# Optimization experiments

Measured on AMD Instinct MI355X. Metric: run time of the kernel, lower is better.

The kernel has to match this reference:

```python
import jax, jax.numpy as jnp
import numpy as np

B, R, C, OUT, IN = 64, 2048, 32, 32, 16
ROUTING_ITERS = 3


def squash(s, axis=-1):
    s_norm = jnp.linalg.norm(s, axis=axis, keepdims=True)
    scale = s_norm ** 2 / (1.0 + s_norm ** 2)
    return scale * s / (s_norm + 1e-8)


def setup_inputs() -> dict:
    key = jax.random.key(0)
    k1, k2 = jax.random.split(key)
    x = jax.random.normal(k1, (B, R, IN), dtype=jnp.float32)
    W = jax.random.normal(k2, (1, R, C, OUT, IN), dtype=jnp.float32)
    return {"x": x, "W": W}


def reference(x, W):
    # u_hat[b,r,c,o] = sum_i W[r,c,o,i] * x[b,r,i]
    u_hat = jnp.einsum('rcoi,bri->brco', W[0], x)  # [B,R,C,OUT]
    b = jnp.zeros((x.shape[0], R, C), dtype=x.dtype)
    v = None
    for i in range(ROUTING_ITERS):
        c = jax.nn.softmax(b, axis=2)[..., None]       # [B,R,C,1]
        s = jnp.sum(c * u_hat, axis=1)                 # [B,C,OUT]
        v = squash(s)                                  # [B,C,OUT]
        if i < ROUTING_ITERS - 1:
            b = b + jnp.einsum('brco,bco->brc', u_hat, v)
    return v
```

## Files before the change

kernel.cpp:

```cpp
#include <hip/hip_runtime.h>


#define Bn 64
#define Rn 2048
#define Cn 32
#define On 32
#define In 16
#define RCH 16
#define NRC2 (Rn / RCH)
#define NG 4

typedef _Float16 half4v __attribute__((ext_vector_type(4)));
typedef float floatx4 __attribute__((ext_vector_type(4)));

__global__ __launch_bounds__(256)
void wconv(const float* __restrict__ W, _Float16* __restrict__ Wh) {
    const size_t i = ((size_t)blockIdx.x * 256 + threadIdx.x) * 8;
    const float4 a = *(const float4*)(W + i);
    const float4 b = *(const float4*)(W + i + 4);
    union { _Float16 h[8]; uint4 u; } pk;
    pk.h[0] = (_Float16)a.x; pk.h[1] = (_Float16)a.y;
    pk.h[2] = (_Float16)a.z; pk.h[3] = (_Float16)a.w;
    pk.h[4] = (_Float16)b.x; pk.h[5] = (_Float16)b.y;
    pk.h[6] = (_Float16)b.z; pk.h[7] = (_Float16)b.w;
    *(uint4*)(Wh + i) = pk.u;
}

template <int PHASE>
__global__ __launch_bounds__(512, 2)
void upass(const float* __restrict__ x, const _Float16* __restrict__ Wh,
           const float* __restrict__ vroute, float* __restrict__ s_part) {
    const int tid  = threadIdx.x;
    const int w    = tid >> 6;
    const int lane = tid & 63;
    const int q    = lane >> 4;
    const int bl   = lane & 15;

    const int L  = blockIdx.x;
    const int bg = (L >> 3) & 3;
    const int rc = (L & 7) | ((L >> 5) << 3);
    const int b0 = bg * 16;

    __shared__ __attribute__((aligned(16))) _Float16 xs[RCH * 16 * 20];
    __shared__ __attribute__((aligned(16))) float vs[(PHASE > 0) ? 16 * 1028 : 4];
    __shared__ __attribute__((aligned(16))) float sums[2][16][8];

#pragma unroll
    for (int k = 0; k < 2; ++k) {
        const int u  = tid + k * 512;
        const int rr = u >> 6, bb = (u >> 2) & 15, iq = u & 3;
        const float4 xv = *(const float4*)(x + (size_t)(b0 + bb) * (Rn * In) +
                                           (size_t)(rc * RCH + rr) * In + iq * 4);
        union { _Float16 h[4]; uint2 u2; } p;
        p.h[0] = (_Float16)xv.x; p.h[1] = (_Float16)xv.y;
        p.h[2] = (_Float16)xv.z; p.h[3] = (_Float16)xv.w;
        *(uint2*)(xs + (rr * 16 + bb) * 20 + iq * 4) = p.u2;
    }
    if constexpr (PHASE > 0) {
#pragma unroll
        for (int k = 0; k < 8; ++k) {
            const int u = tid + k * 512;
            const int bb = u >> 8, off = (u & 255) * 4;
            const float4 vv = *(const float4*)(vroute + (size_t)(b0 + bb) * 1024 + off);
            *(float4*)(vs + bb * 1028 + off) = vv;
        }
    }
    __syncthreads();

    floatx4 accS[8];
#pragma unroll
    for (int m = 0; m < 8; ++m) accS[m] = (floatx4){0.f, 0.f, 0.f, 0.f};

    for (int rr = 0; rr < RCH; ++rr) {
        const int r = rc * RCH + rr;
        const _Float16* Wr = Wh + ((size_t)r * 1024 + w * 128 + bl) * 16 + 4 * q;
        half4v a[8];
#pragma unroll
        for (int m = 0; m < 8; ++m) a[m] = *(const half4v*)(Wr + m * 256);
        const half4v bf = *(const half4v*)(xs + (rr * 16 + bl) * 20 + 4 * q);

        if constexpr (PHASE == 0) {
#pragma unroll
            for (int m = 0; m < 8; ++m)
                accS[m] = __builtin_amdgcn_mfma_f32_16x16x16f16(a[m], bf, accS[m], 0, 0, 0);
        } else {
            floatx4 D[8];
#pragma unroll
            for (int m = 0; m < 8; ++m)
                D[m] = __builtin_amdgcn_mfma_f32_16x16x16f16(
                           a[m], bf, (floatx4){0.f, 0.f, 0.f, 0.f}, 0, 0, 0);

            float e[4], se = 0.f;
#pragma unroll
            for (int t = 0; t < 4; ++t) {
                const int ct = w * 4 + t;
                const float* vp = vs + bl * 1028 + ct * 32 + 4 * q;
                const floatx4 v0 = *(const floatx4*)(vp);
                const floatx4 v1 = *(const floatx4*)(vp + 16);
                float lp = D[2*t].x * v0.x + D[2*t].y * v0.y +
                           D[2*t].z * v0.z + D[2*t].w * v0.w +
                           D[2*t+1].x * v1.x + D[2*t+1].y * v1.y +
                           D[2*t+1].z * v1.z + D[2*t+1].w * v1.w;
                lp += __shfl_xor(lp, 16, 64);
                lp += __shfl_xor(lp, 32, 64);
                e[t] = __expf(lp);
                se += e[t];
            }
            if (lane < 16) sums[rr & 1][bl][w] = se;
            __syncthreads();
            const floatx4 s0 = *(const floatx4*)(&sums[rr & 1][bl][0]);
            const floatx4 s1 = *(const floatx4*)(&sums[rr & 1][bl][4]);
            const float tot = s0.x + s0.y + s0.z + s0.w +
                              s1.x + s1.y + s1.z + s1.w;
            const float winv = __builtin_amdgcn_rcpf(tot);
#pragma unroll
            for (int t = 0; t < 4; ++t) {
                const float wt = e[t] * winv;
                accS[2*t]   += wt * D[2*t];
                accS[2*t+1] += wt * D[2*t+1];
            }
        }
    }

    const size_t sb = (((size_t)rc * 64 + b0 + bl)) * 1024 + w * 128 + 4 * q;
#pragma unroll
    for (int m = 0; m < 8; ++m)
        *(floatx4*)(s_part + sb + m * 16) = accS[m];
}

__global__ __launch_bounds__(256)
void reduce_all(const float* __restrict__ sp, float* __restrict__ s2) {
    const int b = blockIdx.x, t = threadIdx.x;
    floatx4 acc = (floatx4){0.f, 0.f, 0.f, 0.f};
    for (int k = 0; k < NRC2; ++k)
        acc += *(const floatx4*)(sp + ((size_t)k * 64 + b) * 1024 + t * 4);
    *(floatx4*)(s2 + (size_t)b * 1024 + t * 4) = acc;
}

__global__ __launch_bounds__(256)
void squash_v(const float* __restrict__ s2, float scale,
              float* __restrict__ vout, const float* __restrict__ vprev,
              float* __restrict__ vsum) {
    const int b = blockIdx.x, t = threadIdx.x;
    const int c = t >> 3, j = t & 7;
    floatx4 s = *(const floatx4*)(s2 + (size_t)b * 1024 + c * 32 + j * 4);
    s *= scale;
    float n2 = s.x * s.x + s.y * s.y + s.z * s.z + s.w * s.w;
    n2 += __shfl_xor(n2, 1, 64);
    n2 += __shfl_xor(n2, 2, 64);
    n2 += __shfl_xor(n2, 4, 64);
    const float norm = sqrtf(n2);
    const float f = (n2 / (1.f + n2)) / (norm + 1e-8f);
    const floatx4 vv = s * f;
    const size_t o = (size_t)b * 1024 + c * 32 + j * 4;
    if (vout) *(floatx4*)(vout + o) = vv;
    if (vsum) {
        const floatx4 vp = *(const floatx4*)(vprev + o);
        *(floatx4*)(vsum + o) = vv + vp;
    }
}

extern "C" void kernel_launch(void* const* d_in, const int* in_sizes, int n_in,
                              void* d_out, int out_size, void* d_ws, size_t ws_size,
                              hipStream_t stream) {
    const float* x = (const float*)d_in[0];
    const float* W = (const float*)d_in[1];
    float* out = (float*)d_out;

    char* ws = (char*)d_ws;
    _Float16* Wh  = (_Float16*)ws;
    float* s_part = (float*)(ws + (size_t)67108864);
    float* s2     = (float*)(ws + (size_t)67108864 + 33554432);
    float* v1     = (float*)(ws + (size_t)67108864 + 33554432 + 262144);
    float* v12    = (float*)(ws + (size_t)67108864 + 33554432 + 524288);

    const int ublocks = NG * NRC2;

    wconv<<<16384, 256, 0, stream>>>(W, Wh);

    upass<0><<<ublocks, 512, 0, stream>>>(x, Wh, nullptr, s_part);
    reduce_all<<<Bn, 256, 0, stream>>>(s_part, s2);
    squash_v<<<Bn, 256, 0, stream>>>(s2, 1.f / 32.f, v1, nullptr, nullptr);

    upass<1><<<ublocks, 512, 0, stream>>>(x, Wh, v1, s_part);
    reduce_all<<<Bn, 256, 0, stream>>>(s_part, s2);
    squash_v<<<Bn, 256, 0, stream>>>(s2, 1.f, nullptr, v1, v12);

    upass<2><<<ublocks, 512, 0, stream>>>(x, Wh, v12, s_part);
    reduce_all<<<Bn, 256, 0, stream>>>(s_part, s2);
    squash_v<<<Bn, 256, 0, stream>>>(s2, 1.f, out, nullptr, nullptr);
}
```

Before: 315.5 us.

## Fuse reduce and squash, prefetch W into registers, keep v in registers

Merges the partial-sum reduction and the squash into one kernel that spreads each batch row over 8 blocks, with a shared-memory tree step, so more of the GPU works on the reduction and one launch per iteration disappears. In the routing passes, the v vectors move from a large shared-memory staging buffer into per-thread registers, which frees LDS and may raise occupancy. The W fragments and x operand for the next row are now loaded one iteration ahead to overlap global loads with MFMA work. The __syncthreads is also replaced by an explicit LDS waitcnt plus s_barrier. The cost is more register pressure under the 512x2 launch bounds.

Result: no change. 311.4 us (-1.3%).

```diff
diff --git a/kernel.cpp b/kernel.cpp
--- a/kernel.cpp
+++ b/kernel.cpp
@@ -42,8 +42,17 @@
     const int b0 = bg * 16;
 
     __shared__ __attribute__((aligned(16))) _Float16 xs[RCH * 16 * 20];
-    __shared__ __attribute__((aligned(16))) float vs[(PHASE > 0) ? 16 * 1028 : 4];
     __shared__ __attribute__((aligned(16))) float sums[2][16][8];
+
+    floatx4 vr0[4], vr1[4];
+    if constexpr (PHASE > 0) {
+        const float* vb = vroute + (size_t)(b0 + bl) * 1024 + 4 * q;
+#pragma unroll
+        for (int t = 0; t < 4; ++t) {
+            vr0[t] = *(const floatx4*)(vb + (w * 4 + t) * 32);
+            vr1[t] = *(const floatx4*)(vb + (w * 4 + t) * 32 + 16);
+        }
+    }
 
 #pragma unroll
     for (int k = 0; k < 2; ++k) {
@@ -56,33 +65,31 @@
         p.h[2] = (_Float16)xv.z; p.h[3] = (_Float16)xv.w;
         *(uint2*)(xs + (rr * 16 + bb) * 20 + iq * 4) = p.u2;
     }
-    if constexpr (PHASE > 0) {
-#pragma unroll
-        for (int k = 0; k < 8; ++k) {
-            const int u = tid + k * 512;
-            const int bb = u >> 8, off = (u & 255) * 4;
-            const float4 vv = *(const float4*)(vroute + (size_t)(b0 + bb) * 1024 + off);
-            *(float4*)(vs + bb * 1028 + off) = vv;
-        }
-    }
     __syncthreads();
 
     floatx4 accS[8];
 #pragma unroll
     for (int m = 0; m < 8; ++m) accS[m] = (floatx4){0.f, 0.f, 0.f, 0.f};
 
+    const _Float16* Wp = Wh + ((size_t)(rc * RCH) * 1024 + w * 128 + bl) * 16 + 4 * q;
+
+    half4v a[8];
+#pragma unroll
+    for (int m = 0; m < 8; ++m) a[m] = *(const half4v*)(Wp + m * 256);
+    half4v bf = *(const half4v*)(xs + bl * 20 + 4 * q);
+
     for (int rr = 0; rr < RCH; ++rr) {
-        const int r = rc * RCH + rr;
-        const _Float16* Wr = Wh + ((size_t)r * 1024 + w * 128 + bl) * 16 + 4 * q;
-        half4v a[8];
-#pragma unroll
-        for (int m = 0; m < 8; ++m) a[m] = *(const half4v*)(Wr + m * 256);
-        const half4v bf = *(const half4v*)(xs + (rr * 16 + bl) * 20 + 4 * q);
+        const int rn = (rr + 1 < RCH) ? rr + 1 : rr;
+        const _Float16* Wn = Wp + (size_t)rn * 16384;
 
         if constexpr (PHASE == 0) {
 #pragma unroll
             for (int m = 0; m < 8; ++m)
                 accS[m] = __builtin_amdgcn_mfma_f32_16x16x16f16(a[m], bf, accS[m], 0, 0, 0);
+            const half4v bn = *(const half4v*)(xs + (rn * 16 + bl) * 20 + 4 * q);
+#pragma unroll
+            for (int m = 0; m < 8; ++m) a[m] = *(const half4v*)(Wn + m * 256);
+            bf = bn;
         } else {
             floatx4 D[8];
 #pragma unroll
@@ -90,13 +97,16 @@
                 D[m] = __builtin_amdgcn_mfma_f32_16x16x16f16(
                            a[m], bf, (floatx4){0.f, 0.f, 0.f, 0.f}, 0, 0, 0);
 
+            const half4v bn = *(const half4v*)(xs + (rn * 16 + bl) * 20 + 4 * q);
+#pragma unroll
+            for (int m = 0; m < 8; ++m) a[m] = *(const half4v*)(Wn + m * 256);
+            bf = bn;
+
             float e[4], se = 0.f;
 #pragma unroll
             for (int t = 0; t < 4; ++t) {
-                const int ct = w * 4 + t;
-                const float* vp = vs + bl * 1028 + ct * 32 + 4 * q;
-                const floatx4 v0 = *(const floatx4*)(vp);
-                const floatx4 v1 = *(const floatx4*)(vp + 16);
+                const floatx4 v0 = vr0[t];
+                const floatx4 v1 = vr1[t];
                 float lp = D[2*t].x * v0.x + D[2*t].y * v0.y +
                            D[2*t].z * v0.z + D[2*t].w * v0.w +
                            D[2*t+1].x * v1.x + D[2*t+1].y * v1.y +
@@ -107,7 +117,9 @@
                 se += e[t];
             }
             if (lane < 16) sums[rr & 1][bl][w] = se;
-            __syncthreads();
+            asm volatile("s_waitcnt lgkmcnt(0)" ::: "memory");
+            __builtin_amdgcn_s_barrier();
+            asm volatile("" ::: "memory");
             const floatx4 s0 = *(const floatx4*)(&sums[rr & 1][bl][0]);
             const floatx4 s1 = *(const floatx4*)(&sums[rr & 1][bl][4]);
             const float tot = s0.x + s0.y + s0.z + s0.w +
@@ -129,34 +141,40 @@
 }
 
 __global__ __launch_bounds__(256)
-void reduce_all(const float* __restrict__ sp, float* __restrict__ s2) {
-    const int b = blockIdx.x, t = threadIdx.x;
+void reduce_squash(const float* __restrict__ sp, float scale,
+                   float* __restrict__ vout, const float* __restrict__ vprev,
+                   float* __restrict__ vsum) {
+    const int b = blockIdx.x >> 3, oct = blockIdx.x & 7;
+    const int t = threadIdx.x;
+    const int kg = t >> 5, ci = t & 31;
+    const size_t base = (size_t)b * 1024 + (size_t)oct * 128 + (size_t)ci * 4;
+
     floatx4 acc = (floatx4){0.f, 0.f, 0.f, 0.f};
-    for (int k = 0; k < NRC2; ++k)
-        acc += *(const floatx4*)(sp + ((size_t)k * 64 + b) * 1024 + t * 4);
-    *(floatx4*)(s2 + (size_t)b * 1024 + t * 4) = acc;
-}
-
-__global__ __launch_bounds__(256)
-void squash_v(const float* __restrict__ s2, float scale,
-              float* __restrict__ vout, const float* __restrict__ vprev,
-              float* __restrict__ vsum) {
-    const int b = blockIdx.x, t = threadIdx.x;
-    const int c = t >> 3, j = t & 7;
-    floatx4 s = *(const floatx4*)(s2 + (size_t)b * 1024 + c * 32 + j * 4);
-    s *= scale;
-    float n2 = s.x * s.x + s.y * s.y + s.z * s.z + s.w * s.w;
-    n2 += __shfl_xor(n2, 1, 64);
-    n2 += __shfl_xor(n2, 2, 64);
-    n2 += __shfl_xor(n2, 4, 64);
-    const float norm = sqrtf(n2);
-    const float f = (n2 / (1.f + n2)) / (norm + 1e-8f);
-    const floatx4 vv = s * f;
-    const size_t o = (size_t)b * 1024 + c * 32 + j * 4;
-    if (vout) *(floatx4*)(vout + o) = vv;
-    if (vsum) {
-        const floatx4 vp = *(const floatx4*)(vprev + o);
-        *(floatx4*)(vsum + o) = vv + vp;
+#pragma unroll 4
+    for (int k = kg * 16; k < kg * 16 + 16; ++k)
+        acc += *(const floatx4*)(sp + (size_t)k * 65536 + base);
+
+    __shared__ __attribute__((aligned(16))) float red[8][128];
+    *(floatx4*)(&red[kg][ci * 4]) = acc;
+    __syncthreads();
+
+    if (t < 128) {
+        float s = 0.f;
+#pragma unroll
+        for (int g = 0; g < 8; ++g) s += red[g][t];
+        s *= scale;
+        float n2 = s * s;
+        n2 += __shfl_xor(n2, 1, 64);
+        n2 += __shfl_xor(n2, 2, 64);
+        n2 += __shfl_xor(n2, 4, 64);
+        n2 += __shfl_xor(n2, 8, 64);
+        n2 += __shfl_xor(n2, 16, 64);
+        const float norm = sqrtf(n2);
+        const float f = (n2 / (1.f + n2)) / (norm + 1e-8f);
+        const float vv = s * f;
+        const size_t o = (size_t)b * 1024 + (size_t)oct * 128 + t;
+        if (vout) vout[o] = vv;
+        if (vsum) vsum[o] = vv + vprev[o];
     }
 }
 
@@ -170,23 +188,19 @@
     char* ws = (char*)d_ws;
     _Float16* Wh  = (_Float16*)ws;
     float* s_part = (float*)(ws + (size_t)67108864);
-    float* s2     = (float*)(ws + (size_t)67108864 + 33554432);
-    float* v1     = (float*)(ws + (size_t)67108864 + 33554432 + 262144);
-    float* v12    = (float*)(ws + (size_t)67108864 + 33554432 + 524288);
+    float* v1     = (float*)(ws + (size_t)67108864 + 33554432);
+    float* v12    = (float*)(ws + (size_t)67108864 + 33554432 + 262144);
 
     const int ublocks = NG * NRC2;
 
     wconv<<<16384, 256, 0, stream>>>(W, Wh);
 
     upass<0><<<ublocks, 512, 0, stream>>>(x, Wh, nullptr, s_part);
-    reduce_all<<<Bn, 256, 0, stream>>>(s_part, s2);
-    squash_v<<<Bn, 256, 0, stream>>>(s2, 1.f / 32.f, v1, nullptr, nullptr);
+    reduce_squash<<<512, 256, 0, stream>>>(s_part, 1.f / 32.f, v1, nullptr, nullptr);
 
     upass<1><<<ublocks, 512, 0, stream>>>(x, Wh, v1, s_part);
-    reduce_all<<<Bn, 256, 0, stream>>>(s_part, s2);
-    squash_v<<<Bn, 256, 0, stream>>>(s2, 1.f, nullptr, v1, v12);
+    reduce_squash<<<512, 256, 0, stream>>>(s_part, 1.f, nullptr, v1, v12);
 
     upass<2><<<ublocks, 512, 0, stream>>>(x, Wh, v12, s_part);
-    reduce_all<<<Bn, 256, 0, stream>>>(s_part, s2);
-    squash_v<<<Bn, 256, 0, stream>>>(s2, 1.f, out, nullptr, nullptr);
-}
+    reduce_squash<<<512, 256, 0, stream>>>(s_part, 1.f, out, nullptr, nullptr);
+}
```
